# Optimization experiments

Measured on AMD Instinct MI355X. Metric: run time of the kernel, lower is better.

## Reference

```python
import jax, jax.numpy as jnp
import numpy as np

K = 7          # kernel_size
PAD = 3        # padding (same-size output)
GROUPS = 8


def _unfold(z, H, W):
    # z: [B, C, H+2p, W+2p] -> patches [B, C, H, W, K*K], flat index = kh*K + kw
    # matches torch .unfold(2,K,1).unfold(3,K,1).view(..., -1)
    return jnp.stack(
        [z[:, :, a:a + H, b:b + W] for a in range(K) for b in range(K)],
        axis=-1,
    )


def setup_inputs() -> dict:
    key = jax.random.key(0)
    ks = jax.random.split(key, 7)
    B, C, H, W = 4, 64, 64, 64
    Cout = 64
    fan_scale = (2.0 / Cout) ** 0.5  # kaiming fan_out, 1x1 conv
    return {
        "x": jax.random.normal(ks[0], (B, C, H, W), jnp.float32),
        "y": jax.random.normal(ks[1], (B, C, H, W), jnp.float32),
        "Wq": jax.random.normal(ks[2], (Cout, C), jnp.float32) * fan_scale,
        "Wk": jax.random.normal(ks[3], (Cout, C), jnp.float32) * fan_scale,
        "Wv": jax.random.normal(ks[4], (Cout, C), jnp.float32) * fan_scale,
        "rel_h": jax.random.normal(ks[5], (Cout // 2, K), jnp.float32),
        "rel_w": jax.random.normal(ks[6], (Cout // 2, K), jnp.float32),
    }


def reference(x, y, Wq, Wk, Wv, rel_h, rel_w):
    B, C, H, W = x.shape
    Cout = Wq.shape[0]
    half = Cout // 2

    # 1x1 convs (no bias) commute with zero padding, so project first.
    q = jnp.einsum('oc,bchw->bohw', Wq, x)          # [B, Cout, H, W]
    k_full = jnp.einsum('oc,bchw->bohw', Wk, x)
    v_full = jnp.einsum('oc,bchw->bohw', Wv, y)

    pad4 = ((0, 0), (0, 0), (PAD, PAD), (PAD, PAD))
    k_pat = _unfold(jnp.pad(k_full, pad4), H, W)    # [B, Cout, H, W, K*K]
    v_pat = _unfold(jnp.pad(v_full, pad4), H, W)

    # relative-position bias: rel_h over kh (top half of channels), rel_w over kw
    bias_h = jnp.broadcast_to(rel_h[:, :, None], (half, K, K))   # [Cout/2, kh, kw]
    bias_w = jnp.broadcast_to(rel_w[:, None, :], (half, K, K))
    bias = jnp.concatenate([bias_h, bias_w], axis=0).reshape(Cout, K * K)
    k_pat = k_pat + bias[None, :, None, None, :]

    cg = Cout // GROUPS
    k_pat = k_pat.reshape(B, GROUPS, cg, H, W, K * K)
    v_pat = v_pat.reshape(B, GROUPS, cg, H, W, K * K)
    q = q.reshape(B, GROUPS, cg, H, W, 1)

    attn = jax.nn.softmax(q * k_pat, axis=-1)       # per-channel softmax over window
    out = jnp.sum(attn * v_pat, axis=-1)            # [B, G, cg, H, W]
    return out.reshape(B, Cout, H, W)
```

## Files before the change

kernel.cpp:

```cpp
#include <hip/hip_runtime.h>

#define HW 4096

typedef float f4 __attribute__((ext_vector_type(4)));
typedef float f2 __attribute__((ext_vector_type(2)));

#define WSTRIDE 194

__global__ __launch_bounds__(256) void proj_kernel(
    const float* __restrict__ x, const float* __restrict__ y,
    const float* __restrict__ Wq, const float* __restrict__ Wk,
    const float* __restrict__ Wv,
    float* __restrict__ qkv)
{
    __shared__ float lds[64 * WSTRIDE];
    const int t = threadIdx.x;

    {
        const float* Ws[3] = {Wq, Wk, Wv};
#pragma unroll
        for (int m = 0; m < 3; ++m) {
#pragma unroll
            for (int s = 0; s < 4; ++s) {
                const int fi = s * 256 + t;
                const int co = fi >> 4, c4 = fi & 15;
                const f4 w = *(const f4*)&Ws[m][co * 64 + c4 * 4];
#pragma unroll
                for (int i = 0; i < 4; ++i)
                    lds[(c4 * 4 + i) * WSTRIDE + m * 64 + co] = w[i];
            }
        }
    }
    __syncthreads();

    const int cg  = t & 31;
    const int pq  = t >> 5;
    const int px0 = blockIdx.x * 64;
    const int b   = px0 >> 12;
    const int poffb = px0 & 4095;
    const int poff  = poffb + pq * 8;
    const float* xb = x + (size_t)b * 64 * HW + poff;
    const float* yb = y + (size_t)b * 64 * HW + poff;

    f4 acc[3][2][2];
#pragma unroll
    for (int m = 0; m < 3; ++m)
#pragma unroll
        for (int i = 0; i < 2; ++i)
#pragma unroll
            for (int h = 0; h < 2; ++h)
                acc[m][i][h] = (f4){0.f, 0.f, 0.f, 0.f};

#pragma unroll 8
    for (int c = 0; c < 64; ++c) {
        const f4 xv0 = *(const f4*)&xb[c * HW];
        const f4 xv1 = *(const f4*)&xb[c * HW + 4];
        const f4 yv0 = *(const f4*)&yb[c * HW];
        const f4 yv1 = *(const f4*)&yb[c * HW + 4];
        const float* wr = &lds[c * WSTRIDE + 2 * cg];
        const f2 wq = *(const f2*)&wr[0];
        const f2 wk = *(const f2*)&wr[64];
        const f2 wv = *(const f2*)&wr[128];
        acc[0][0][0] += xv0 * wq[0];  acc[0][0][1] += xv1 * wq[0];
        acc[0][1][0] += xv0 * wq[1];  acc[0][1][1] += xv1 * wq[1];
        acc[1][0][0] += xv0 * wk[0];  acc[1][0][1] += xv1 * wk[0];
        acc[1][1][0] += xv0 * wk[1];  acc[1][1][1] += xv1 * wk[1];
        acc[2][0][0] += yv0 * wv[0];  acc[2][0][1] += yv1 * wv[0];
        acc[2][1][0] += yv0 * wv[1];  acc[2][1][1] += yv1 * wv[1];
    }

    __syncthreads();

#pragma unroll
    for (int m = 0; m < 3; ++m)
#pragma unroll
        for (int i = 0; i < 2; ++i)
#pragma unroll
            for (int h = 0; h < 2; ++h) {
                const int row = m * 64 + 2 * cg + i;
                const int ch  = pq * 2 + h;
                *(f4*)&lds[row * 64 + ((ch ^ (row & 15)) << 2)] = acc[m][i][h];
            }
    __syncthreads();

#pragma unroll
    for (int s = 0; s < 12; ++s) {
        const int fi  = s * 256 + t;
        const int row = fi >> 4, ch = fi & 15;
        const f4 val = *(const f4*)&lds[row * 64 + ((ch ^ (row & 15)) << 2)];
        float* dst = qkv + (size_t)(row >> 6) * (1 << 20)
                         + ((size_t)b * 64 + (row & 63)) * HW + poffb + ch * 4;
        *(f4*)dst = val;
    }
}

__global__ __launch_bounds__(256) void attn_kernel(
    const float* __restrict__ qg, const float* __restrict__ kg,
    const float* __restrict__ vg,
    const float* __restrict__ rel_h, const float* __restrict__ rel_w,
    float* __restrict__ out)
{
    __shared__ float kT[22 * 72];
    __shared__ float vT[22 * 72];

    const int blk = blockIdx.x;
    const int bc  = blk >> 2;
    const int h0  = (blk & 3) << 4;
    const int c   = bc & 63;
    const int t   = threadIdx.x;

    const float* kimg = kg + (size_t)bc * HW;
    const float* vimg = vg + (size_t)bc * HW;
    const f4 z4 = {0.f, 0.f, 0.f, 0.f};

    if (t < 88) {
        const int row = t >> 2, side = (t >> 1) & 1, arr = t & 1;
        float* dst = arr ? vT : kT;
        *(f4*)&dst[row * 72 + side * 68] = z4;
    }
#pragma unroll
    for (int j = 0; j < 2; ++j) {
        const int idx = j * 256 + t;
        if (idx < 352) {
            const int row = idx >> 4, ch = idx & 15;
            const int hy = h0 - 3 + row;
            const bool rv = ((unsigned)hy < 64u);
            const f4 kv = rv ? *(const f4*)&kimg[hy * 64 + ch * 4] : z4;
            const f4 vv = rv ? *(const f4*)&vimg[hy * 64 + ch * 4] : z4;
            *(f4*)&kT[row * 72 + ch * 4 + 4] = kv;
            *(f4*)&vT[row * 72 + ch * 4 + 4] = vv;
        }
    }
    __syncthreads();

    const int r  = t >> 4;
    const int w0 = (t & 15) << 2;
    const int h  = h0 + r;

    const float LOG2E = 1.4426950408889634f;
    const f4 qv = *(const f4*)&qg[(size_t)bc * HW + h * 64 + w0];
    float qe[4];
#pragma unroll
    for (int p = 0; p < 4; ++p) qe[p] = qv[p] * LOG2E;

    float qb[7][4];
    if (c < 32) {
#pragma unroll
        for (int a = 0; a < 7; ++a) {
            const float bb = rel_h[c * 7 + a];
#pragma unroll
            for (int p = 0; p < 4; ++p) qb[a][p] = qe[p] * bb;
        }
    } else {
#pragma unroll
        for (int j = 0; j < 7; ++j) {
            const float bb = rel_w[(c - 32) * 7 + j];
#pragma unroll
            for (int p = 0; p < 4; ++p) qb[j][p] = qe[p] * bb;
        }
    }

    float l[4] = {0.f, 0.f, 0.f, 0.f};
    float o[4] = {0.f, 0.f, 0.f, 0.f};

    if (c < 32) {
#pragma unroll
        for (int a = 0; a < 7; ++a) {
            const int ro = (r + a) * 72 + w0;
            const f4 k0 = *(const f4*)&kT[ro];
            const f4 k1 = *(const f4*)&kT[ro + 4];
            const f4 k2 = *(const f4*)&kT[ro + 8];
            const f4 v0 = *(const f4*)&vT[ro];
            const f4 v1 = *(const f4*)&vT[ro + 4];
            const f4 v2 = *(const f4*)&vT[ro + 8];
            const float kw[12] = {k0[0], k0[1], k0[2], k0[3], k1[0], k1[1], k1[2], k1[3],
                                  k2[0], k2[1], k2[2], k2[3]};
            const float vw[12] = {v0[0], v0[1], v0[2], v0[3], v1[0], v1[1], v1[2], v1[3],
                                  v2[0], v2[1], v2[2], v2[3]};
#pragma unroll
            for (int b2 = 0; b2 < 7; ++b2)
#pragma unroll
                for (int p = 0; p < 4; ++p) {
                    const float s = fmaf(qe[p], kw[p + b2 + 1], qb[a][p]);
                    const float e = __builtin_amdgcn_exp2f(s);
                    l[p] += e;
                    o[p] = fmaf(e, vw[p + b2 + 1], o[p]);
                }
        }
    } else {
#pragma unroll
        for (int a = 0; a < 7; ++a) {
            const int ro = (r + a) * 72 + w0;
            const f4 k0 = *(const f4*)&kT[ro];
            const f4 k1 = *(const f4*)&kT[ro + 4];
            const f4 k2 = *(const f4*)&kT[ro + 8];
            const f4 v0 = *(const f4*)&vT[ro];
            const f4 v1 = *(const f4*)&vT[ro + 4];
            const f4 v2 = *(const f4*)&vT[ro + 8];
            const float kw[12] = {k0[0], k0[1], k0[2], k0[3], k1[0], k1[1], k1[2], k1[3],
                                  k2[0], k2[1], k2[2], k2[3]};
            const float vw[12] = {v0[0], v0[1], v0[2], v0[3], v1[0], v1[1], v1[2], v1[3],
                                  v2[0], v2[1], v2[2], v2[3]};
#pragma unroll
            for (int b2 = 0; b2 < 7; ++b2)
#pragma unroll
                for (int p = 0; p < 4; ++p) {
                    const float s = fmaf(qe[p], kw[p + b2 + 1], qb[b2][p]);
                    const float e = __builtin_amdgcn_exp2f(s);
                    l[p] += e;
                    o[p] = fmaf(e, vw[p + b2 + 1], o[p]);
                }
        }
    }

    f4 res;
#pragma unroll
    for (int p = 0; p < 4; ++p)
        res[p] = o[p] * __builtin_amdgcn_rcpf(l[p]);
    *(f4*)&out[(size_t)bc * HW + h * 64 + w0] = res;
}

extern "C" void kernel_launch(void* const* d_in, const int* in_sizes, int n_in,
                              void* d_out, int out_size, void* d_ws, size_t ws_size,
                              hipStream_t stream) {
    const float* x   = (const float*)d_in[0];
    const float* y   = (const float*)d_in[1];
    const float* Wq  = (const float*)d_in[2];
    const float* Wk  = (const float*)d_in[3];
    const float* Wv  = (const float*)d_in[4];
    const float* rlh = (const float*)d_in[5];
    const float* rlw = (const float*)d_in[6];
    float* out = (float*)d_out;

    float* qkv = (float*)d_ws;
    float* q = qkv;
    float* k = qkv + (1 << 20);
    float* v = qkv + (2 << 20);

    proj_kernel<<<256, 256, 0, stream>>>(x, y, Wq, Wk, Wv, qkv);
    attn_kernel<<<1024, 256, 0, stream>>>(q, k, v, rlh, rlw, out);
}
```

Before: 106.1 us.

## Restructure projection kernel into one pixel per thread with uniform weight loads

Replaces the LDS-staged, register-tiled projection kernel with a simple kernel that launches 3072 single-wave blocks. Each thread loads its pixel's 64 input channels into registers and computes 16 output channels of one projection, reading weights as wave-uniform (likely scalar) loads. This removes the LDS staging, the barriers and the transpose-through-LDS for the output, and adds more blocks for parallelism. In exchange, x is re-read 8 times and y 4 times across blocks, and stores become scalar per thread. Each thread also holds 64 floats in registers.

```diff
diff --git a/kernel.cpp b/kernel.cpp
--- a/kernel.cpp
+++ b/kernel.cpp
@@ -3,94 +3,40 @@
 #define HW 4096
 
 typedef float f4 __attribute__((ext_vector_type(4)));
-typedef float f2 __attribute__((ext_vector_type(2)));
 
-#define WSTRIDE 194
-
-__global__ __launch_bounds__(256) void proj_kernel(
+__global__ __launch_bounds__(64) void proj_kernel(
     const float* __restrict__ x, const float* __restrict__ y,
     const float* __restrict__ Wq, const float* __restrict__ Wk,
     const float* __restrict__ Wv,
     float* __restrict__ qkv)
 {
-    __shared__ float lds[64 * WSTRIDE];
-    const int t = threadIdx.x;
+    const int blk = blockIdx.x;
+    const int pc  = blk & 255;
+    const int sp  = blk >> 8;
+    const int m   = sp >> 2;
+    const int cb  = (sp & 3) << 4;
+    const int px  = pc * 64 + threadIdx.x;
+    const int b   = px >> 12;
+    const int pp  = px & 4095;
 
-    {
-        const float* Ws[3] = {Wq, Wk, Wv};
+    const float* W   = (m == 0) ? Wq : (m == 1) ? Wk : Wv;
+    const float* src = (m == 2) ? y : x;
+    const float* sb  = src + (size_t)b * 64 * HW + pp;
+
+    float xv[64];
 #pragma unroll
-        for (int m = 0; m < 3; ++m) {
+    for (int c = 0; c < 64; ++c)
+        xv[c] = sb[c * HW];
+
+    float* dstm = qkv + (size_t)m * (1 << 20) + (size_t)b * 64 * HW + pp;
 #pragma unroll
-            for (int s = 0; s < 4; ++s) {
-                const int fi = s * 256 + t;
-                const int co = fi >> 4, c4 = fi & 15;
-                const f4 w = *(const f4*)&Ws[m][co * 64 + c4 * 4];
+    for (int i = 0; i < 16; ++i) {
+        const float* wr = W + (cb + i) * 64;
+        float acc = 0.f;
 #pragma unroll
-                for (int i = 0; i < 4; ++i)
-                    lds[(c4 * 4 + i) * WSTRIDE + m * 64 + co] = w[i];
-            }
-        }
-    }
-    __syncthreads();
-
-    const int cg  = t & 31;
-    const int pq  = t >> 5;
-    const int px0 = blockIdx.x * 64;
-    const int b   = px0 >> 12;
-    const int poffb = px0 & 4095;
-    const int poff  = poffb + pq * 8;
-    const float* xb = x + (size_t)b * 64 * HW + poff;
-    const float* yb = y + (size_t)b * 64 * HW + poff;
-
-    f4 acc[3][2][2];
-#pragma unroll
-    for (int m = 0; m < 3; ++m)
-#pragma unroll
-        for (int i = 0; i < 2; ++i)
-#pragma unroll
-            for (int h = 0; h < 2; ++h)
-                acc[m][i][h] = (f4){0.f, 0.f, 0.f, 0.f};
-
-#pragma unroll 8
-    for (int c = 0; c < 64; ++c) {
-        const f4 xv0 = *(const f4*)&xb[c * HW];
-        const f4 xv1 = *(const f4*)&xb[c * HW + 4];
-        const f4 yv0 = *(const f4*)&yb[c * HW];
-        const f4 yv1 = *(const f4*)&yb[c * HW + 4];
-        const float* wr = &lds[c * WSTRIDE + 2 * cg];
-        const f2 wq = *(const f2*)&wr[0];
-        const f2 wk = *(const f2*)&wr[64];
-        const f2 wv = *(const f2*)&wr[128];
-        acc[0][0][0] += xv0 * wq[0];  acc[0][0][1] += xv1 * wq[0];
-        acc[0][1][0] += xv0 * wq[1];  acc[0][1][1] += xv1 * wq[1];
-        acc[1][0][0] += xv0 * wk[0];  acc[1][0][1] += xv1 * wk[0];
-        acc[1][1][0] += xv0 * wk[1];  acc[1][1][1] += xv1 * wk[1];
-        acc[2][0][0] += yv0 * wv[0];  acc[2][0][1] += yv1 * wv[0];
-        acc[2][1][0] += yv0 * wv[1];  acc[2][1][1] += yv1 * wv[1];
-    }
-
-    __syncthreads();
-
-#pragma unroll
-    for (int m = 0; m < 3; ++m)
-#pragma unroll
-        for (int i = 0; i < 2; ++i)
-#pragma unroll
-            for (int h = 0; h < 2; ++h) {
-                const int row = m * 64 + 2 * cg + i;
-                const int ch  = pq * 2 + h;
-                *(f4*)&lds[row * 64 + ((ch ^ (row & 15)) << 2)] = acc[m][i][h];
-            }
-    __syncthreads();
-
-#pragma unroll
-    for (int s = 0; s < 12; ++s) {
-        const int fi  = s * 256 + t;
-        const int row = fi >> 4, ch = fi & 15;
-        const f4 val = *(const f4*)&lds[row * 64 + ((ch ^ (row & 15)) << 2)];
-        float* dst = qkv + (size_t)(row >> 6) * (1 << 20)
-                         + ((size_t)b * 64 + (row & 63)) * HW + poffb + ch * 4;
-        *(f4*)dst = val;
+        for (int c = 0; c < 64; ++c)
+            acc = fmaf(wr[c], xv[c], acc);
+        dstm[(size_t)(cb + i) * HW] = acc;
     }
 }
 
@@ -237,6 +183,6 @@
     float* k = qkv + (1 << 20);
     float* v = qkv + (2 << 20);
 
-    proj_kernel<<<256, 256, 0, stream>>>(x, y, Wq, Wk, Wv, qkv);
+    proj_kernel<<<3072, 64, 0, stream>>>(x, y, Wq, Wk, Wv, qkv);
     attn_kernel<<<1024, 256, 0, stream>>>(q, k, v, rlh, rlw, out);
 }
```

Result: no change. 104.2 us (-1.8%).
